# Kernel tuning notes

Measured on AMD Instinct MI355X. Metric: run time of the kernel, lower is better.

Reference implementation:

```python
import jax, jax.numpy as jnp
import numpy as np

N = 50000      # nodes
E = 800000     # edges
IN_DIM = 128
HID = 16       # per-head hidden dim (layer1)
HEADS = 8
OUT_DIM = 32   # layer2 output dim (1 head)
NEG_SLOPE = 0.2  # GAT-paper LeakyReLU slope


def _gat_layer(x, W, a_src, a_dst, src, dst, num_nodes):
    """One multi-head GAT layer.
    x: [N, Fin]; W: [Fin, H*D]; a_src/a_dst: [H, D]; src/dst: [E].
    Returns [N, H, D].
    """
    H, D = a_src.shape
    z = (x @ W).reshape(num_nodes, H, D)            # [N, H, D]
    # edge attention logits: attn_fc([z_src || z_dst]) split into two dots
    e_s = jnp.einsum('nhd,hd->nh', z, a_src)        # [N, H]
    e_d = jnp.einsum('nhd,hd->nh', z, a_dst)        # [N, H]
    e = e_s[src] + e_d[dst]                          # [E, H]
    e = jnp.where(e >= 0, e, NEG_SLOPE * e)          # leaky_relu
    # softmax over incoming edges of each destination node
    m = jax.ops.segment_max(e, dst, num_segments=num_nodes)   # [N, H]
    ex = jnp.exp(e - m[dst])                                   # [E, H]
    s = jax.ops.segment_sum(ex, dst, num_segments=num_nodes)  # [N, H]
    alpha = ex / s[dst]                                        # [E, H]
    msg = alpha[:, :, None] * z[src]                            # [E, H, D]
    return jax.ops.segment_sum(msg, dst, num_segments=num_nodes)  # [N, H, D]


def setup_inputs() -> dict:
    key = jax.random.key(0)
    ks = jax.random.split(key, 9)
    h = jax.random.normal(ks[0], (N, IN_DIM), dtype=jnp.float32)
    src = jax.random.randint(ks[1], (E,), 0, N, dtype=jnp.int32)
    dst = jax.random.randint(ks[2], (E,), 0, N, dtype=jnp.int32)
    sc1 = 1.0 / np.sqrt(IN_DIM)
    W1 = jax.random.normal(ks[3], (IN_DIM, HEADS * HID), dtype=jnp.float32) * sc1
    a1_src = jax.random.normal(ks[4], (HEADS, HID), dtype=jnp.float32) * 0.1
    a1_dst = jax.random.normal(ks[5], (HEADS, HID), dtype=jnp.float32) * 0.1
    sc2 = 1.0 / np.sqrt(HEADS * HID)
    W2 = jax.random.normal(ks[6], (HEADS * HID, OUT_DIM), dtype=jnp.float32) * sc2
    a2_src = jax.random.normal(ks[7], (1, OUT_DIM), dtype=jnp.float32) * 0.1
    a2_dst = jax.random.normal(ks[8], (1, OUT_DIM), dtype=jnp.float32) * 0.1
    return {"h": h, "W1": W1, "a1_src": a1_src, "a1_dst": a1_dst,
            "W2": W2, "a2_src": a2_src, "a2_dst": a2_dst,
            "src": src, "dst": dst}


def reference(h, W1, a1_src, a1_dst, W2, a2_src, a2_dst, src, dst):
    # layer1: multi-head, concat heads -> [N, HEADS*HID]
    h1 = _gat_layer(h, W1, a1_src, a1_dst, src, dst, N).reshape(N, HEADS * HID)
    h1 = jax.nn.elu(h1)
    # layer2: single head -> [N, OUT_DIM]
    out = _gat_layer(h1, W2, a2_src, a2_dst, src, dst, N).reshape(N, OUT_DIM)
    return out
```

## Files before the change

kernel.cpp:

```cpp
#include <hip/hip_runtime.h>
#include <hip/hip_fp16.h>
#include <math.h>

#define NN 50000
#define EE 800000
#define FIN 128
#define F1  128
#define NH  8
#define DH  16
#define F2  32
#define SLOPE 0.2f
#define LOG2E 1.44269504f

#define EB 4096
#define NBLK ((EE + EB - 1) / EB)
#define BK  391
#define SEGCAP 4096

typedef _Float16 f16x8 __attribute__((ext_vector_type(8)));
typedef float    f32x4 __attribute__((ext_vector_type(4)));

__global__ __launch_bounds__(256) void hist_kernel(const int* __restrict__ dst,
        int* __restrict__ hist) {
    __shared__ int lc[BK];
    int tid = threadIdx.x;
    for (int i = tid; i < BK; i += 256) lc[i] = 0;
    __syncthreads();
    int base = blockIdx.x * EB;
    int end = base + EB; if (end > EE) end = EE;
    for (int i = base + tid; i < end; i += 256)
        atomicAdd(&lc[dst[i] >> 7], 1);
    __syncthreads();
    for (int i = tid; i < BK; i += 256)
        if (lc[i]) atomicAdd(&hist[i], lc[i]);
}

__global__ __launch_bounds__(256) void scan_hist_kernel(const int* __restrict__ hist,
        int* __restrict__ basea, int* __restrict__ cursor) {
    __shared__ int sh[256];
    int tid = threadIdx.x;
    int a0 = hist[2 * tid], a1 = hist[2 * tid + 1];
    int tsum = a0 + a1;
    sh[tid] = tsum;
    __syncthreads();
    for (int off = 1; off < 256; off <<= 1) {
        int t = (tid >= off) ? sh[tid - off] : 0;
        __syncthreads();
        sh[tid] += t;
        __syncthreads();
    }
    int ex = sh[tid] - tsum;
    basea[2 * tid] = ex;     cursor[2 * tid] = ex;
    basea[2 * tid + 1] = ex + a0; cursor[2 * tid + 1] = ex + a0;
}

__global__ __launch_bounds__(256) void split_kernel(const int* __restrict__ src,
        const int* __restrict__ dst, int* __restrict__ cursor, unsigned int* __restrict__ sorted) {
    __shared__ int lc[512];
    __shared__ int lofs[512];
    __shared__ int lcur[BK];
    __shared__ int delta[BK];
    __shared__ int sh[256];
    __shared__ unsigned int recs[EB];
    __shared__ unsigned short rbk[EB];
    int tid = threadIdx.x;
    for (int i = tid; i < 512; i += 256) lc[i] = 0;
    __syncthreads();
    int base = blockIdx.x * EB;
    int cnt = EE - base; if (cnt > EB) cnt = EB;
    unsigned int myrec[16];
    #pragma unroll
    for (int k = 0; k < 16; ++k) {
        int i = base + tid + k * 256;
        myrec[k] = 0xFFFFFFFFu;
        if (i - base < cnt) {
            unsigned int d = (unsigned int)dst[i];
            myrec[k] = (d << 16) | (unsigned int)src[i];
            atomicAdd(&lc[d >> 7], 1);
        }
    }
    __syncthreads();
    int a0 = lc[2 * tid], a1 = lc[2 * tid + 1];
    int tsum = a0 + a1;
    sh[tid] = tsum;
    __syncthreads();
    for (int off = 1; off < 256; off <<= 1) {
        int t = (tid >= off) ? sh[tid - off] : 0;
        __syncthreads();
        sh[tid] += t;
        __syncthreads();
    }
    int ex = sh[tid] - tsum;
    lofs[2 * tid] = ex;
    lofs[2 * tid + 1] = ex + a0;
    __syncthreads();
    for (int b = tid; b < BK; b += 256) {
        int c = lc[b];
        lcur[b] = lofs[b];
        if (c) {
            int g = atomicAdd(&cursor[b], c);
            delta[b] = g - lofs[b];
        }
    }
    __syncthreads();
    #pragma unroll
    for (int k = 0; k < 16; ++k) {
        if (myrec[k] != 0xFFFFFFFFu) {
            int b = (int)(myrec[k] >> 23);
            int pos = atomicAdd(&lcur[b], 1);
            recs[pos] = myrec[k];
            rbk[pos] = (unsigned short)b;
        }
    }
    __syncthreads();
    for (int s = tid; s < cnt; s += 256)
        sorted[s + delta[rbk[s]]] = recs[s];
}

__global__ __launch_bounds__(256) void csrbuild_kernel(const int* __restrict__ basea,
        const unsigned int* __restrict__ sorted, unsigned short* __restrict__ csr,
        int* __restrict__ row_ptr) {
    __shared__ unsigned int recs[SEGCAP];
    __shared__ unsigned short csr_sh[SEGCAP];
    __shared__ int ncnt[128], nofs[128], ncur[128];
    __shared__ int sh[256];
    int b = blockIdx.x;
    int tid = threadIdx.x;
    int s0 = basea[b], s1 = basea[b + 1];
    int cnt = s1 - s0; if (cnt > SEGCAP) cnt = SEGCAP;
    if (tid < 128) ncnt[tid] = 0;
    __syncthreads();
    for (int i = tid; i < cnt; i += 256) {
        unsigned int r = sorted[s0 + i];
        recs[i] = r;
        atomicAdd(&ncnt[(r >> 16) & 127], 1);
    }
    __syncthreads();
    int v = (tid < 128) ? ncnt[tid] : 0;
    sh[tid] = v;
    __syncthreads();
    for (int off = 1; off < 256; off <<= 1) {
        int t = (tid >= off) ? sh[tid - off] : 0;
        __syncthreads();
        sh[tid] += t;
        __syncthreads();
    }
    int ex = sh[tid] - v;
    if (tid < 128) {
        nofs[tid] = ex;
        ncur[tid] = ex;
        int node = b * 128 + tid;
        if (node < NN) row_ptr[node] = s0 + ex;
    }
    if (b == BK - 1 && tid == 0) row_ptr[NN] = EE;
    __syncthreads();
    for (int i = tid; i < cnt; i += 256) {
        unsigned int r = recs[i];
        int local = (r >> 16) & 127;
        int p = atomicAdd(&ncur[local], 1);
        csr_sh[p] = (unsigned short)(r & 0xFFFFu);
    }
    __syncthreads();
    for (int i = tid; i < cnt; i += 256)
        csr[s0 + i] = csr_sh[i];
}

__global__ __launch_bounds__(256) void gemm1_kernel(const float* __restrict__ h,
        const float* __restrict__ W, const float* __restrict__ a1s, const float* __restrict__ a1d,
        __half* __restrict__ z1h, float* __restrict__ es1x, float* __restrict__ ed1x) {
    __shared__ alignas(16) __half hs[64 * 136];
    __shared__ alignas(16) __half wls[128 * 136];
    int tid = threadIdx.x;
    for (int idx = tid; idx < FIN * F1; idx += 256) {
        int k = idx >> 7, n = idx & 127;
        wls[n * 136 + k] = __float2half(W[idx]);
    }
    int rowBase = blockIdx.x * 64;
    for (int idx4 = tid; idx4 < 64 * 32; idx4 += 256) {
        int r = idx4 >> 5, cc = (idx4 & 31) * 4;
        int n = rowBase + r;
        float4 v = (n < NN) ? *(const float4*)&h[(size_t)n * FIN + cc] : make_float4(0, 0, 0, 0);
        union { __half2 h2[2]; int2 i; } u;
        u.h2[0] = __floats2half2_rn(v.x, v.y);
        u.h2[1] = __floats2half2_rn(v.z, v.w);
        *(int2*)&hs[r * 136 + cc] = u.i;
    }
    __syncthreads();
    int l = tid & 63, w = tid >> 6;
    int q = l >> 4, cl = l & 15;
    int m0 = w * 16;
    float as[8], ad[8];
    #pragma unroll
    for (int t = 0; t < 8; ++t) { as[t] = a1s[t * DH + cl]; ad[t] = a1d[t * DH + cl]; }
    f32x4 acc[8];
    #pragma unroll
    for (int t = 0; t < 8; ++t) acc[t] = (f32x4){0.f, 0.f, 0.f, 0.f};
    const __half* ap = &hs[(m0 + cl) * 136 + q * 8];
    const __half* bp = &wls[cl * 136 + q * 8];
    #pragma unroll
    for (int k0 = 0; k0 < 128; k0 += 32) {
        f16x8 af = *(const f16x8*)(ap + k0);
        #pragma unroll
        for (int t = 0; t < 8; ++t) {
            f16x8 bf = *(const f16x8*)(bp + t * 16 * 136 + k0);
            acc[t] = __builtin_amdgcn_mfma_f32_16x16x32_f16(af, bf, acc[t], 0, 0, 0);
        }
    }
    #pragma unroll
    for (int t = 0; t < 8; ++t) {
        #pragma unroll
        for (int reg = 0; reg < 4; ++reg) {
            int row = rowBase + m0 + q * 4 + reg;
            float z = acc[t][reg];
            float s = z * as[t], d = z * ad[t];
            s += __shfl_xor(s, 1, 64); d += __shfl_xor(d, 1, 64);
            s += __shfl_xor(s, 2, 64); d += __shfl_xor(d, 2, 64);
            s += __shfl_xor(s, 4, 64); d += __shfl_xor(d, 4, 64);
            s += __shfl_xor(s, 8, 64); d += __shfl_xor(d, 8, 64);
            if (row < NN) {
                z1h[(size_t)row * F1 + t * 16 + cl] = __float2half(z);
                if (cl == 0) {
                    es1x[row * NH + t] = s * LOG2E;
                    ed1x[row * NH + t] = d * LOG2E;
                }
            }
        }
    }
}

__global__ __launch_bounds__(256) void gemm2_kernel(const __half* __restrict__ h1h,
        const float* __restrict__ W, const float* __restrict__ a2s, const float* __restrict__ a2d,
        __half* __restrict__ z2h, float* __restrict__ es2x, float* __restrict__ ed2x) {
    __shared__ alignas(16) __half hs[64 * 136];
    __shared__ alignas(16) __half wls[32 * 136];
    int tid = threadIdx.x;
    for (int idx = tid; idx < FIN * F2; idx += 256) {
        int k = idx >> 5, n = idx & 31;
        wls[n * 136 + k] = __float2half(W[idx]);
    }
    int rowBase = blockIdx.x * 64;
    for (int idx8 = tid; idx8 < 64 * 16; idx8 += 256) {
        int r = idx8 >> 4, cc = (idx8 & 15) * 8;
        int n = rowBase + r;
        float4 v = make_float4(0, 0, 0, 0);
        if (n < NN) v = *(const float4*)&h1h[(size_t)n * FIN + cc];
        *(float4*)&hs[r * 136 + cc] = v;
    }
    __syncthreads();
    int l = tid & 63, w = tid >> 6;
    int q = l >> 4, cl = l & 15;
    int m0 = w * 16;
    float as0 = a2s[cl], as1 = a2s[16 + cl];
    float ad0 = a2d[cl], ad1 = a2d[16 + cl];
    f32x4 acc[2];
    acc[0] = (f32x4){0.f, 0.f, 0.f, 0.f};
    acc[1] = (f32x4){0.f, 0.f, 0.f, 0.f};
    const __half* ap = &hs[(m0 + cl) * 136 + q * 8];
    const __half* bp = &wls[cl * 136 + q * 8];
    #pragma unroll
    for (int k0 = 0; k0 < 128; k0 += 32) {
        f16x8 af = *(const f16x8*)(ap + k0);
        #pragma unroll
        for (int t = 0; t < 2; ++t) {
            f16x8 bf = *(const f16x8*)(bp + t * 16 * 136 + k0);
            acc[t] = __builtin_amdgcn_mfma_f32_16x16x32_f16(af, bf, acc[t], 0, 0, 0);
        }
    }
    #pragma unroll
    for (int reg = 0; reg < 4; ++reg) {
        int row = rowBase + m0 + q * 4 + reg;
        float s = acc[0][reg] * as0 + acc[1][reg] * as1;
        float d = acc[0][reg] * ad0 + acc[1][reg] * ad1;
        s += __shfl_xor(s, 1, 64); d += __shfl_xor(d, 1, 64);
        s += __shfl_xor(s, 2, 64); d += __shfl_xor(d, 2, 64);
        s += __shfl_xor(s, 4, 64); d += __shfl_xor(d, 4, 64);
        s += __shfl_xor(s, 8, 64); d += __shfl_xor(d, 8, 64);
        if (row < NN) {
            z2h[(size_t)row * F2 + cl]      = __float2half(acc[0][reg]);
            z2h[(size_t)row * F2 + 16 + cl] = __float2half(acc[1][reg]);
            if (cl == 0) {
                es2x[row] = s * LOG2E;
                ed2x[row] = d * LOG2E;
            }
        }
    }
}

__global__ __launch_bounds__(256) void attn1_kernel(const int* __restrict__ row_ptr,
        const unsigned short* __restrict__ csr, const __half* __restrict__ z1h,
        const float* __restrict__ es, const float* __restrict__ ed,
        __half* __restrict__ h1h) {
    int gt = blockIdx.x * 256 + threadIdx.x;
    int n = gt >> 4;
    int j = gt & 15;
    int hl = j >> 1;
    if (n >= NN) return;
    int b0 = row_ptr[n];
    int cnt = row_ptr[n + 1] - b0;
    float edn = ed[n * NH + hl];
    float acc[8] = {0.f, 0.f, 0.f, 0.f, 0.f, 0.f, 0.f, 0.f};
    float ws = 0.f;
    for (int i = 0; i < cnt; ++i) {
        int s = csr[b0 + i];
        float e = es[s * NH + hl] + edn;
        e = e >= 0.f ? e : SLOPE * e;
        float wv = exp2f(e);
        ws += wv;
        union { float4 f; __half2 h2[4]; } u;
        u.f = *(const float4*)&z1h[(size_t)s * F1 + j * 8];
        #pragma unroll
        for (int t = 0; t < 4; ++t) {
            float2 v = __half22float2(u.h2[t]);
            acc[2*t]   = fmaf(wv, v.x, acc[2*t]);
            acc[2*t+1] = fmaf(wv, v.y, acc[2*t+1]);
        }
    }
    float rs = ws > 0.f ? 1.0f / ws : 0.f;
    union { float4 f; __half2 h2[4]; } p;
    #pragma unroll
    for (int t = 0; t < 4; ++t) {
        float x0 = acc[2*t] * rs, x1 = acc[2*t+1] * rs;
        x0 = x0 > 0.f ? x0 : __expf(x0) - 1.0f;
        x1 = x1 > 0.f ? x1 : __expf(x1) - 1.0f;
        p.h2[t] = __floats2half2_rn(x0, x1);
    }
    *(float4*)&h1h[(size_t)n * F1 + j * 8] = p.f;
}

__global__ __launch_bounds__(256) void attn2_kernel(const int* __restrict__ row_ptr,
        const unsigned short* __restrict__ csr, const __half* __restrict__ z2h,
        const float* __restrict__ es, const float* __restrict__ ed,
        float* __restrict__ out) {
    int gt = blockIdx.x * 256 + threadIdx.x;
    int n = gt >> 2;
    int j = gt & 3;
    if (n >= NN) return;
    int b0 = row_ptr[n];
    int cnt = row_ptr[n + 1] - b0;
    float edn = ed[n];
    float acc[8] = {0.f, 0.f, 0.f, 0.f, 0.f, 0.f, 0.f, 0.f};
    float ws = 0.f;
    for (int i = 0; i < cnt; ++i) {
        int s = csr[b0 + i];
        float e = es[s] + edn;
        e = e >= 0.f ? e : SLOPE * e;
        float wv = exp2f(e);
        ws += wv;
        union { float4 f; __half2 h2[4]; } u;
        u.f = *(const float4*)&z2h[(size_t)s * F2 + j * 8];
        #pragma unroll
        for (int t = 0; t < 4; ++t) {
            float2 v = __half22float2(u.h2[t]);
            acc[2*t]   = fmaf(wv, v.x, acc[2*t]);
            acc[2*t+1] = fmaf(wv, v.y, acc[2*t+1]);
        }
    }
    float rs = ws > 0.f ? 1.0f / ws : 0.f;
    float* op = &out[(size_t)n * F2 + j * 8];
    *(float4*)&op[0] = make_float4(acc[0]*rs, acc[1]*rs, acc[2]*rs, acc[3]*rs);
    *(float4*)&op[4] = make_float4(acc[4]*rs, acc[5]*rs, acc[6]*rs, acc[7]*rs);
}

extern "C" void kernel_launch(void* const* d_in, const int* in_sizes, int n_in,
                              void* d_out, int out_size, void* d_ws, size_t ws_size,
                              hipStream_t stream) {
    const float* h   = (const float*)d_in[0];
    const float* W1  = (const float*)d_in[1];
    const float* a1s = (const float*)d_in[2];
    const float* a1d = (const float*)d_in[3];
    const float* W2  = (const float*)d_in[4];
    const float* a2s = (const float*)d_in[5];
    const float* a2d = (const float*)d_in[6];
    const int*   src = (const int*)d_in[7];
    const int*   dst = (const int*)d_in[8];
    float* out = (float*)d_out;

    int* ip      = (int*)d_ws;
    int* hist    = ip;
    int* basea   = hist + 512;
    int* cursor  = basea + 520;
    int* row_ptr = cursor + 512;
    unsigned int* sorted = (unsigned int*)(row_ptr + NN + 8);
    unsigned short* csr16 = (unsigned short*)(sorted + EE);
    float* es1x = (float*)(csr16 + EE);
    float* ed1x = es1x + (size_t)NN * NH;
    float* es2x = ed1x + (size_t)NN * NH;
    float* ed2x = es2x + NN;
    __half* z1h = (__half*)(ed2x + NN);
    __half* h1h = z1h + (size_t)NN * F1;
    __half* z2h = h1h + (size_t)NN * F1;

    hipMemsetAsync(hist, 0, 512 * sizeof(int), stream);

    hist_kernel<<<NBLK, 256, 0, stream>>>(dst, hist);
    scan_hist_kernel<<<1, 256, 0, stream>>>(hist, basea, cursor);
    split_kernel<<<NBLK, 256, 0, stream>>>(src, dst, cursor, sorted);
    csrbuild_kernel<<<BK, 256, 0, stream>>>(basea, sorted, csr16, row_ptr);

    int gb = (NN + 63) / 64;
    gemm1_kernel<<<gb, 256, 0, stream>>>(h, W1, a1s, a1d, z1h, es1x, ed1x);
    attn1_kernel<<<(NN * 16 + 255) / 256, 256, 0, stream>>>(row_ptr, csr16, z1h, es1x, ed1x, h1h);
    gemm2_kernel<<<gb, 256, 0, stream>>>(h1h, W2, a2s, a2d, z2h, es2x, ed2x);
    attn2_kernel<<<(NN * 4 + 255) / 256, 256, 0, stream>>>(row_ptr, csr16, z2h, es2x, ed2x, out);
}
```

Baseline: 217.5 us.

## Merge CSR build stages with GEMM1, pre-transpose weights, unroll edge gather loops

The histogram kernel now also transposes W1 and W2 into fp16 once, in extra blocks. The split kernel is merged with gemm1 into one heterogeneous launch, so the edge bucketing and the dense projection run concurrently. The separate single-block scan is dropped: each block recomputes the bucket prefix scan from the histogram. The attention gather loops are unrolled by 8 so more neighbour loads are in flight at once. Together these cut launch count and serial dependencies, in exchange for redundant scans and a larger dynamic shared-memory footprint in the fused kernel.

New measurement: 201.5 us. -7.3%, faster.

```diff
diff --git a/kernel.cpp b/kernel.cpp
--- a/kernel.cpp
+++ b/kernel.cpp
@@ -16,120 +16,206 @@
 #define NBLK ((EE + EB - 1) / EB)
 #define BK  391
 #define SEGCAP 4096
+#define PREPB 80
+#define GEMM1B ((NN + 63) / 64)
 
 typedef _Float16 f16x8 __attribute__((ext_vector_type(8)));
 typedef float    f32x4 __attribute__((ext_vector_type(4)));
 
-__global__ __launch_bounds__(256) void hist_kernel(const int* __restrict__ dst,
-        int* __restrict__ hist) {
-    __shared__ int lc[BK];
+__global__ __launch_bounds__(256) void k1_hist_prep(const int* __restrict__ dst,
+        const float* __restrict__ W1, const float* __restrict__ W2,
+        __half* __restrict__ wt1, __half* __restrict__ wt2, int* __restrict__ hist) {
     int tid = threadIdx.x;
-    for (int i = tid; i < BK; i += 256) lc[i] = 0;
-    __syncthreads();
-    int base = blockIdx.x * EB;
-    int end = base + EB; if (end > EE) end = EE;
-    for (int i = base + tid; i < end; i += 256)
-        atomicAdd(&lc[dst[i] >> 7], 1);
-    __syncthreads();
-    for (int i = tid; i < BK; i += 256)
-        if (lc[i]) atomicAdd(&hist[i], lc[i]);
-}
-
-__global__ __launch_bounds__(256) void scan_hist_kernel(const int* __restrict__ hist,
-        int* __restrict__ basea, int* __restrict__ cursor) {
-    __shared__ int sh[256];
+    if (blockIdx.x < NBLK) {
+        __shared__ int lc[BK];
+        for (int i = tid; i < BK; i += 256) lc[i] = 0;
+        __syncthreads();
+        int base = blockIdx.x * EB;
+        int end = base + EB; if (end > EE) end = EE;
+        for (int i = base + tid; i < end; i += 256)
+            atomicAdd(&lc[dst[i] >> 7], 1);
+        __syncthreads();
+        for (int i = tid; i < BK; i += 256)
+            if (lc[i]) atomicAdd(&hist[i], lc[i]);
+    } else {
+        int gidx = (blockIdx.x - NBLK) * 256 + tid;
+        if (gidx < FIN * F1) {
+            int n = gidx >> 7, k = gidx & 127;
+            wt1[gidx] = __float2half(W1[k * F1 + n]);
+        } else {
+            int t2 = gidx - FIN * F1;
+            if (t2 < F2 * FIN) {
+                int n = t2 >> 7, k = t2 & 127;
+                wt2[t2] = __float2half(W2[k * F2 + n]);
+            }
+        }
+    }
+}
+
+extern __shared__ char smem_k2[];
+__global__ __launch_bounds__(256) void k2_split_gemm1(const int* __restrict__ src,
+        const int* __restrict__ dst, const int* __restrict__ hist, int* __restrict__ cursor,
+        unsigned int* __restrict__ sorted,
+        const float* __restrict__ h, const __half* __restrict__ wt1,
+        const float* __restrict__ a1s, const float* __restrict__ a1d,
+        __half* __restrict__ z1h, float* __restrict__ es1x, float* __restrict__ ed1x) {
     int tid = threadIdx.x;
-    int a0 = hist[2 * tid], a1 = hist[2 * tid + 1];
-    int tsum = a0 + a1;
-    sh[tid] = tsum;
-    __syncthreads();
-    for (int off = 1; off < 256; off <<= 1) {
-        int t = (tid >= off) ? sh[tid - off] : 0;
-        __syncthreads();
-        sh[tid] += t;
-        __syncthreads();
-    }
-    int ex = sh[tid] - tsum;
-    basea[2 * tid] = ex;     cursor[2 * tid] = ex;
-    basea[2 * tid + 1] = ex + a0; cursor[2 * tid + 1] = ex + a0;
-}
-
-__global__ __launch_bounds__(256) void split_kernel(const int* __restrict__ src,
-        const int* __restrict__ dst, int* __restrict__ cursor, unsigned int* __restrict__ sorted) {
-    __shared__ int lc[512];
-    __shared__ int lofs[512];
-    __shared__ int lcur[BK];
-    __shared__ int delta[BK];
-    __shared__ int sh[256];
-    __shared__ unsigned int recs[EB];
-    __shared__ unsigned short rbk[EB];
-    int tid = threadIdx.x;
-    for (int i = tid; i < 512; i += 256) lc[i] = 0;
-    __syncthreads();
-    int base = blockIdx.x * EB;
-    int cnt = EE - base; if (cnt > EB) cnt = EB;
-    unsigned int myrec[16];
-    #pragma unroll
-    for (int k = 0; k < 16; ++k) {
-        int i = base + tid + k * 256;
-        myrec[k] = 0xFFFFFFFFu;
-        if (i - base < cnt) {
-            unsigned int d = (unsigned int)dst[i];
-            myrec[k] = (d << 16) | (unsigned int)src[i];
-            atomicAdd(&lc[d >> 7], 1);
-        }
-    }
-    __syncthreads();
-    int a0 = lc[2 * tid], a1 = lc[2 * tid + 1];
-    int tsum = a0 + a1;
-    sh[tid] = tsum;
-    __syncthreads();
-    for (int off = 1; off < 256; off <<= 1) {
-        int t = (tid >= off) ? sh[tid - off] : 0;
-        __syncthreads();
-        sh[tid] += t;
-        __syncthreads();
-    }
-    int ex = sh[tid] - tsum;
-    lofs[2 * tid] = ex;
-    lofs[2 * tid + 1] = ex + a0;
-    __syncthreads();
-    for (int b = tid; b < BK; b += 256) {
-        int c = lc[b];
-        lcur[b] = lofs[b];
-        if (c) {
-            int g = atomicAdd(&cursor[b], c);
-            delta[b] = g - lofs[b];
-        }
-    }
-    __syncthreads();
-    #pragma unroll
-    for (int k = 0; k < 16; ++k) {
-        if (myrec[k] != 0xFFFFFFFFu) {
-            int b = (int)(myrec[k] >> 23);
-            int pos = atomicAdd(&lcur[b], 1);
-            recs[pos] = myrec[k];
-            rbk[pos] = (unsigned short)b;
-        }
-    }
-    __syncthreads();
-    for (int s = tid; s < cnt; s += 256)
-        sorted[s + delta[rbk[s]]] = recs[s];
-}
-
-__global__ __launch_bounds__(256) void csrbuild_kernel(const int* __restrict__ basea,
+    if (blockIdx.x < NBLK) {
+        unsigned int*   recs = (unsigned int*)smem_k2;
+        unsigned short* rbk  = (unsigned short*)(smem_k2 + 16384);
+        int* lc    = (int*)(smem_k2 + 24576);
+        int* lofs  = (int*)(smem_k2 + 26624);
+        int* lcur  = (int*)(smem_k2 + 28672);
+        int* delta = (int*)(smem_k2 + 30720);
+        int* bscan = (int*)(smem_k2 + 32768);
+        int* sh    = (int*)(smem_k2 + 34816);
+        for (int i = tid; i < 512; i += 256) lc[i] = 0;
+        __syncthreads();
+        int base = blockIdx.x * EB;
+        int cnt = EE - base; if (cnt > EB) cnt = EB;
+        unsigned int myrec[16];
+        #pragma unroll
+        for (int k = 0; k < 16; ++k) {
+            int i = base + tid + k * 256;
+            myrec[k] = 0xFFFFFFFFu;
+            if (i - base < cnt) {
+                unsigned int d = (unsigned int)dst[i];
+                myrec[k] = (d << 16) | (unsigned int)src[i];
+                atomicAdd(&lc[d >> 7], 1);
+            }
+        }
+        __syncthreads();
+        int a0 = lc[2 * tid], a1 = lc[2 * tid + 1];
+        int tsum = a0 + a1;
+        sh[tid] = tsum;
+        __syncthreads();
+        for (int off = 1; off < 256; off <<= 1) {
+            int t = (tid >= off) ? sh[tid - off] : 0;
+            __syncthreads(); sh[tid] += t; __syncthreads();
+        }
+        int ex = sh[tid] - tsum;
+        lofs[2 * tid] = ex;
+        lofs[2 * tid + 1] = ex + a0;
+        __syncthreads();
+        int h0 = hist[2 * tid], h1 = hist[2 * tid + 1];
+        int hsum = h0 + h1;
+        sh[tid] = hsum;
+        __syncthreads();
+        for (int off = 1; off < 256; off <<= 1) {
+            int t = (tid >= off) ? sh[tid - off] : 0;
+            __syncthreads(); sh[tid] += t; __syncthreads();
+        }
+        int hex = sh[tid] - hsum;
+        bscan[2 * tid] = hex;
+        bscan[2 * tid + 1] = hex + h0;
+        __syncthreads();
+        for (int b = tid; b < BK; b += 256) {
+            int c = lc[b];
+            lcur[b] = lofs[b];
+            if (c) {
+                int g = atomicAdd(&cursor[b], c);
+                delta[b] = bscan[b] + g - lofs[b];
+            }
+        }
+        __syncthreads();
+        #pragma unroll
+        for (int k = 0; k < 16; ++k) {
+            if (myrec[k] != 0xFFFFFFFFu) {
+                int b = (int)(myrec[k] >> 23);
+                int pos = atomicAdd(&lcur[b], 1);
+                recs[pos] = myrec[k];
+                rbk[pos] = (unsigned short)b;
+            }
+        }
+        __syncthreads();
+        for (int s = tid; s < cnt; s += 256)
+            sorted[s + delta[rbk[s]]] = recs[s];
+    } else {
+        __half* hs  = (__half*)smem_k2;
+        __half* wls = (__half*)(smem_k2 + 17408);
+        for (int c = tid; c < 2048; c += 256) {
+            int row = c >> 4, ch = c & 15;
+            *(float4*)&wls[row * 136 + ch * 8] = *(const float4*)&wt1[row * 128 + ch * 8];
+        }
+        int rowBase = (blockIdx.x - NBLK) * 64;
+        for (int idx4 = tid; idx4 < 64 * 32; idx4 += 256) {
+            int r = idx4 >> 5, cc = (idx4 & 31) * 4;
+            int n = rowBase + r;
+            float4 v = (n < NN) ? *(const float4*)&h[(size_t)n * FIN + cc] : make_float4(0, 0, 0, 0);
+            union { __half2 h2[2]; int2 i; } u;
+            u.h2[0] = __floats2half2_rn(v.x, v.y);
+            u.h2[1] = __floats2half2_rn(v.z, v.w);
+            *(int2*)&hs[r * 136 + cc] = u.i;
+        }
+        __syncthreads();
+        int l = tid & 63, w = tid >> 6;
+        int q = l >> 4, cl = l & 15;
+        int m0 = w * 16;
+        float as[8], ad[8];
+        #pragma unroll
+        for (int t = 0; t < 8; ++t) { as[t] = a1s[t * DH + cl]; ad[t] = a1d[t * DH + cl]; }
+        f32x4 acc[8];
+        #pragma unroll
+        for (int t = 0; t < 8; ++t) acc[t] = (f32x4){0.f, 0.f, 0.f, 0.f};
+        const __half* ap = &hs[(m0 + cl) * 136 + q * 8];
+        const __half* bp = &wls[cl * 136 + q * 8];
+        #pragma unroll
+        for (int k0 = 0; k0 < 128; k0 += 32) {
+            f16x8 af = *(const f16x8*)(ap + k0);
+            #pragma unroll
+            for (int t = 0; t < 8; ++t) {
+                f16x8 bf = *(const f16x8*)(bp + t * 16 * 136 + k0);
+                acc[t] = __builtin_amdgcn_mfma_f32_16x16x32_f16(af, bf, acc[t], 0, 0, 0);
+            }
+        }
+        #pragma unroll
+        for (int t = 0; t < 8; ++t) {
+            #pragma unroll
+            for (int reg = 0; reg < 4; ++reg) {
+                int row = rowBase + m0 + q * 4 + reg;
+                float z = acc[t][reg];
+                float s = z * as[t], d = z * ad[t];
+                s += __shfl_xor(s, 1, 64); d += __shfl_xor(d, 1, 64);
+                s += __shfl_xor(s, 2, 64); d += __shfl_xor(d, 2, 64);
+                s += __shfl_xor(s, 4, 64); d += __shfl_xor(d, 4, 64);
+                s += __shfl_xor(s, 8, 64); d += __shfl_xor(d, 8, 64);
+                if (row < NN) {
+                    z1h[(size_t)row * F1 + t * 16 + cl] = __float2half(z);
+                    if (cl == 0) {
+                        es1x[row * NH + t] = s * LOG2E;
+                        ed1x[row * NH + t] = d * LOG2E;
+                    }
+                }
+            }
+        }
+    }
+}
+
+__global__ __launch_bounds__(256) void csrbuild_kernel(const int* __restrict__ hist,
         const unsigned int* __restrict__ sorted, unsigned short* __restrict__ csr,
         int* __restrict__ row_ptr) {
     __shared__ unsigned int recs[SEGCAP];
     __shared__ unsigned short csr_sh[SEGCAP];
-    __shared__ int ncnt[128], nofs[128], ncur[128];
+    __shared__ int ncnt[128], ncur[128];
     __shared__ int sh[256];
+    __shared__ int bscan[512];
     int b = blockIdx.x;
     int tid = threadIdx.x;
-    int s0 = basea[b], s1 = basea[b + 1];
+    int h0 = hist[2 * tid], h1 = hist[2 * tid + 1];
+    int hsum = h0 + h1;
+    sh[tid] = hsum;
+    if (tid < 128) ncnt[tid] = 0;
+    __syncthreads();
+    for (int off = 1; off < 256; off <<= 1) {
+        int t = (tid >= off) ? sh[tid - off] : 0;
+        __syncthreads(); sh[tid] += t; __syncthreads();
+    }
+    int hex = sh[tid] - hsum;
+    bscan[2 * tid] = hex;
+    bscan[2 * tid + 1] = hex + h0;
+    __syncthreads();
+    int s0 = bscan[b], s1 = bscan[b + 1];
     int cnt = s1 - s0; if (cnt > SEGCAP) cnt = SEGCAP;
-    if (tid < 128) ncnt[tid] = 0;
-    __syncthreads();
     for (int i = tid; i < cnt; i += 256) {
         unsigned int r = sorted[s0 + i];
         recs[i] = r;
@@ -141,13 +227,10 @@
     __syncthreads();
     for (int off = 1; off < 256; off <<= 1) {
         int t = (tid >= off) ? sh[tid - off] : 0;
-        __syncthreads();
-        sh[tid] += t;
-        __syncthreads();
+        __syncthreads(); sh[tid] += t; __syncthreads();
     }
     int ex = sh[tid] - v;
     if (tid < 128) {
-        nofs[tid] = ex;
         ncur[tid] = ex;
         int node = b * 128 + tid;
         if (node < NN) row_ptr[node] = s0 + ex;
@@ -165,78 +248,15 @@
         csr[s0 + i] = csr_sh[i];
 }
 
-__global__ __launch_bounds__(256) void gemm1_kernel(const float* __restrict__ h,
-        const float* __restrict__ W, const float* __restrict__ a1s, const float* __restrict__ a1d,
-        __half* __restrict__ z1h, float* __restrict__ es1x, float* __restrict__ ed1x) {
-    __shared__ alignas(16) __half hs[64 * 136];
-    __shared__ alignas(16) __half wls[128 * 136];
-    int tid = threadIdx.x;
-    for (int idx = tid; idx < FIN * F1; idx += 256) {
-        int k = idx >> 7, n = idx & 127;
-        wls[n * 136 + k] = __float2half(W[idx]);
-    }
-    int rowBase = blockIdx.x * 64;
-    for (int idx4 = tid; idx4 < 64 * 32; idx4 += 256) {
-        int r = idx4 >> 5, cc = (idx4 & 31) * 4;
-        int n = rowBase + r;
-        float4 v = (n < NN) ? *(const float4*)&h[(size_t)n * FIN + cc] : make_float4(0, 0, 0, 0);
-        union { __half2 h2[2]; int2 i; } u;
-        u.h2[0] = __floats2half2_rn(v.x, v.y);
-        u.h2[1] = __floats2half2_rn(v.z, v.w);
-        *(int2*)&hs[r * 136 + cc] = u.i;
-    }
-    __syncthreads();
-    int l = tid & 63, w = tid >> 6;
-    int q = l >> 4, cl = l & 15;
-    int m0 = w * 16;
-    float as[8], ad[8];
-    #pragma unroll
-    for (int t = 0; t < 8; ++t) { as[t] = a1s[t * DH + cl]; ad[t] = a1d[t * DH + cl]; }
-    f32x4 acc[8];
-    #pragma unroll
-    for (int t = 0; t < 8; ++t) acc[t] = (f32x4){0.f, 0.f, 0.f, 0.f};
-    const __half* ap = &hs[(m0 + cl) * 136 + q * 8];
-    const __half* bp = &wls[cl * 136 + q * 8];
-    #pragma unroll
-    for (int k0 = 0; k0 < 128; k0 += 32) {
-        f16x8 af = *(const f16x8*)(ap + k0);
-        #pragma unroll
-        for (int t = 0; t < 8; ++t) {
-            f16x8 bf = *(const f16x8*)(bp + t * 16 * 136 + k0);
-            acc[t] = __builtin_amdgcn_mfma_f32_16x16x32_f16(af, bf, acc[t], 0, 0, 0);
-        }
-    }
-    #pragma unroll
-    for (int t = 0; t < 8; ++t) {
-        #pragma unroll
-        for (int reg = 0; reg < 4; ++reg) {
-            int row = rowBase + m0 + q * 4 + reg;
-            float z = acc[t][reg];
-            float s = z * as[t], d = z * ad[t];
-            s += __shfl_xor(s, 1, 64); d += __shfl_xor(d, 1, 64);
-            s += __shfl_xor(s, 2, 64); d += __shfl_xor(d, 2, 64);
-            s += __shfl_xor(s, 4, 64); d += __shfl_xor(d, 4, 64);
-            s += __shfl_xor(s, 8, 64); d += __shfl_xor(d, 8, 64);
-            if (row < NN) {
-                z1h[(size_t)row * F1 + t * 16 + cl] = __float2half(z);
-                if (cl == 0) {
-                    es1x[row * NH + t] = s * LOG2E;
-                    ed1x[row * NH + t] = d * LOG2E;
-                }
-            }
-        }
-    }
-}
-
 __global__ __launch_bounds__(256) void gemm2_kernel(const __half* __restrict__ h1h,
-        const float* __restrict__ W, const float* __restrict__ a2s, const float* __restrict__ a2d,
+        const __half* __restrict__ wt2, const float* __restrict__ a2s, const float* __restrict__ a2d,
         __half* __restrict__ z2h, float* __restrict__ es2x, float* __restrict__ ed2x) {
     __shared__ alignas(16) __half hs[64 * 136];
     __shared__ alignas(16) __half wls[32 * 136];
     int tid = threadIdx.x;
-    for (int idx = tid; idx < FIN * F2; idx += 256) {
-        int k = idx >> 5, n = idx & 31;
-        wls[n * 136 + k] = __float2half(W[idx]);
+    for (int c = tid; c < 512; c += 256) {
+        int row = c >> 4, ch = c & 15;
+        *(float4*)&wls[row * 136 + ch * 8] = *(const float4*)&wt2[row * 128 + ch * 8];
     }
     int rowBase = blockIdx.x * 64;
     for (int idx8 = tid; idx8 < 64 * 16; idx8 += 256) {
@@ -300,11 +320,35 @@
     float edn = ed[n * NH + hl];
     float acc[8] = {0.f, 0.f, 0.f, 0.f, 0.f, 0.f, 0.f, 0.f};
     float ws = 0.f;
-    for (int i = 0; i < cnt; ++i) {
+    int i = 0;
+    for (; i + 8 <= cnt; i += 8) {
+        int ss[8];
+        #pragma unroll
+        for (int u = 0; u < 8; ++u) ss[u] = csr[b0 + i + u];
+        union { float4 f; __half2 h2[4]; } uu[8];
+        #pragma unroll
+        for (int u = 0; u < 8; ++u) uu[u].f = *(const float4*)&z1h[(size_t)ss[u] * F1 + j * 8];
+        float ww[8];
+        #pragma unroll
+        for (int u = 0; u < 8; ++u) {
+            float e = es[ss[u] * NH + hl] + edn;
+            ww[u] = exp2f(e >= 0.f ? e : SLOPE * e);
+            ws += ww[u];
+        }
+        #pragma unroll
+        for (int t = 0; t < 4; ++t) {
+            #pragma unroll
+            for (int u = 0; u < 8; ++u) {
+                float2 v = __half22float2(uu[u].h2[t]);
+                acc[2*t]   = fmaf(ww[u], v.x, acc[2*t]);
+                acc[2*t+1] = fmaf(ww[u], v.y, acc[2*t+1]);
+            }
+        }
+    }
+    for (; i < cnt; ++i) {
         int s = csr[b0 + i];
         float e = es[s * NH + hl] + edn;
-        e = e >= 0.f ? e : SLOPE * e;
-        float wv = exp2f(e);
+        float wv = exp2f(e >= 0.f ? e : SLOPE * e);
         ws += wv;
         union { float4 f; __half2 h2[4]; } u;
         u.f = *(const float4*)&z1h[(size_t)s * F1 + j * 8];
@@ -340,11 +384,35 @@
     float edn = ed[n];
     float acc[8] = {0.f, 0.f, 0.f, 0.f, 0.f, 0.f, 0.f, 0.f};
     float ws = 0.f;
-    for (int i = 0; i < cnt; ++i) {
+    int i = 0;
+    for (; i + 8 <= cnt; i += 8) {
+        int ss[8];
+        #pragma unroll
+        for (int u = 0; u < 8; ++u) ss[u] = csr[b0 + i + u];
+        union { float4 f; __half2 h2[4]; } uu[8];
+        #pragma unroll
+        for (int u = 0; u < 8; ++u) uu[u].f = *(const float4*)&z2h[(size_t)ss[u] * F2 + j * 8];
+        float ww[8];
+        #pragma unroll
+        for (int u = 0; u < 8; ++u) {
+            float e = es[ss[u]] + edn;
+            ww[u] = exp2f(e >= 0.f ? e : SLOPE * e);
+            ws += ww[u];
+        }
+        #pragma unroll
+        for (int t = 0; t < 4; ++t) {
+            #pragma unroll
+            for (int u = 0; u < 8; ++u) {
+                float2 v = __half22float2(uu[u].h2[t]);
+                acc[2*t]   = fmaf(ww[u], v.x, acc[2*t]);
+                acc[2*t+1] = fmaf(ww[u], v.y, acc[2*t+1]);
+            }
+        }
+    }
+    for (; i < cnt; ++i) {
         int s = csr[b0 + i];
         float e = es[s] + edn;
-        e = e >= 0.f ? e : SLOPE * e;
-        float wv = exp2f(e);
+        float wv = exp2f(e >= 0.f ? e : SLOPE * e);
         ws += wv;
         union { float4 f; __half2 h2[4]; } u;
         u.f = *(const float4*)&z2h[(size_t)s * F2 + j * 8];
@@ -377,8 +445,7 @@
 
     int* ip      = (int*)d_ws;
     int* hist    = ip;
-    int* basea   = hist + 512;
-    int* cursor  = basea + 520;
+    int* cursor  = hist + 512;
     int* row_ptr = cursor + 512;
     unsigned int* sorted = (unsigned int*)(row_ptr + NN + 8);
     unsigned short* csr16 = (unsigned short*)(sorted + EE);
@@ -389,17 +456,16 @@
     __half* z1h = (__half*)(ed2x + NN);
     __half* h1h = z1h + (size_t)NN * F1;
     __half* z2h = h1h + (size_t)NN * F1;
-
-    hipMemsetAsync(hist, 0, 512 * sizeof(int), stream);
-
-    hist_kernel<<<NBLK, 256, 0, stream>>>(dst, hist);
-    scan_hist_kernel<<<1, 256, 0, stream>>>(hist, basea, cursor);
-    split_kernel<<<NBLK, 256, 0, stream>>>(src, dst, cursor, sorted);
-    csrbuild_kernel<<<BK, 256, 0, stream>>>(basea, sorted, csr16, row_ptr);
-
-    int gb = (NN + 63) / 64;
-    gemm1_kernel<<<gb, 256, 0, stream>>>(h, W1, a1s, a1d, z1h, es1x, ed1x);
+    __half* wt1 = z2h + (size_t)NN * F2;
+    __half* wt2 = wt1 + FIN * F1;
+
+    hipMemsetAsync(hist, 0, 1024 * sizeof(int), stream);
+
+    k1_hist_prep<<<NBLK + PREPB, 256, 0, stream>>>(dst, W1, W2, wt1, wt2, hist);
+    k2_split_gemm1<<<NBLK + GEMM1B, 256, 52224, stream>>>(src, dst, hist, cursor, sorted,
+                                                          h, wt1, a1s, a1d, z1h, es1x, ed1x);
+    csrbuild_kernel<<<BK, 256, 0, stream>>>(hist, sorted, csr16, row_ptr);
     attn1_kernel<<<(NN * 16 + 255) / 256, 256, 0, stream>>>(row_ptr, csr16, z1h, es1x, ed1x, h1h);
-    gemm2_kernel<<<gb, 256, 0, stream>>>(h1h, W2, a2s, a2d, z2h, es2x, ed2x);
+    gemm2_kernel<<<GEMM1B, 256, 0, stream>>>(h1h, wt2, a2s, a2d, z2h, es2x, ed2x);
     attn2_kernel<<<(NN * 4 + 255) / 256, 256, 0, stream>>>(row_ptr, csr16, z2h, es2x, ed2x, out);
 }
```
